# Performance work log

Measured on AMD Instinct MI355X. Metric: run time of the kernel, lower is better.

Reference implementation:

```python
import jax, jax.numpy as jnp
import numpy as np

N = 50000        # nodes
E = 1_600_000    # edges
G = 64           # graphs in batch
IN = 10          # raw node feature width
XS, XE = 4, 10   # bus slice -> in_dim = 6
H = 256          # hidden_dim
OUT = 256        # out_dim
L = 3            # n_layers per expert
NE = 8           # n_experts
K = 2            # top_k


def _w(key, shape):
    fan_in = shape[-2] if len(shape) > 1 else shape[-1]
    return jax.random.normal(key, shape, jnp.float32) / np.sqrt(fan_in).astype(np.float32)


def setup_inputs() -> dict:
    key = jax.random.key(0)
    ks = jax.random.split(key, 18)
    x = jax.random.normal(ks[0], (N, IN), jnp.float32)
    edge_index = jax.random.randint(ks[1], (2, E), 0, N, dtype=jnp.int32)
    batch = jnp.sort(jax.random.randint(ks[2], (N,), 0, G, dtype=jnp.int32))
    return {
        "x": x,
        "edge_index": edge_index,
        "batch": batch,
        # SharedBusEncoder: Linear(in_dim, hidden) + ReLU
        "W_enc": _w(ks[3], (XE - XS, H)), "b_enc": jnp.zeros((H,), jnp.float32),
        # semantic BaseRouter: Linear(H,H)+ReLU+Linear(H,NE)
        "Ws1": _w(ks[4], (H, H)), "bs1": jnp.zeros((H,), jnp.float32),
        "Ws2": _w(ks[5], (H, NE)), "bs2": jnp.zeros((NE,), jnp.float32),
        # structural BaseRouter: Linear(2,H)+ReLU+Linear(H,NE)
        "Wt1": _w(ks[6], (2, H)), "bt1": jnp.zeros((H,), jnp.float32),
        "Wt2": _w(ks[7], (H, NE)), "bt2": jnp.zeros((NE,), jnp.float32),
        # GraphConvExpert stacks: x' = x@W_self + (sum_neighbors x)@W_neigh + b
        "W_self": _w(ks[8], (NE, L, H, OUT)),
        "W_neigh": _w(ks[9], (NE, L, H, OUT)),
        "b_exp": jnp.zeros((NE, L, OUT), jnp.float32),
    }


def reference(x, edge_index, batch, W_enc, b_enc, Ws1, bs1, Ws2, bs2,
              Wt1, bt1, Wt2, bt2, W_self, W_neigh, b_exp):
    src, dst = edge_index[0], edge_index[1]

    # SharedBusEncoder on bus feature slice
    h = jax.nn.relu(x[:, XS:XE] @ W_enc + b_enc)                       # [N, H]

    # graph_size_features: per-graph log node/edge counts, broadcast to nodes
    nodes_per_g = jax.ops.segment_sum(jnp.ones((N,), jnp.float32), batch, G)
    edges_per_g = jax.ops.segment_sum(jnp.ones((E,), jnp.float32), batch[src], G)
    size_feat = jnp.stack([jnp.log1p(nodes_per_g), jnp.log1p(edges_per_g)], -1)[batch]  # [N, 2]

    # dual routers, averaged
    sem = jax.nn.relu(h @ Ws1 + bs1) @ Ws2 + bs2                       # [N, NE]
    stru = jax.nn.relu(size_feat @ Wt1 + bt1) @ Wt2 + bt2              # [N, NE]
    logits = 0.5 * sem + 0.5 * stru

    # sparse_routing: softmax -> top-k mask -> renormalize (eval path, no noise)
    probs = jax.nn.softmax(logits, axis=-1)
    _, topi = jax.lax.top_k(probs, K)                                  # [N, K]
    mask = jnp.zeros_like(probs).at[jnp.arange(N)[:, None], topi].set(1.0)
    sp = probs * mask
    sparse = sp / jnp.sum(sp, axis=-1, keepdims=True)                  # [N, NE]

    # dense GraphConv experts over all nodes
    def run_expert(Ws, Wn, b):
        z = h
        for l in range(L):
            agg = jax.ops.segment_sum(z[src], dst, N)                  # neighbor sum
            z = z @ Ws[l] + agg @ Wn[l] + b[l]
            if l < L - 1:
                z = jax.nn.relu(z)
        return z                                                        # [N, OUT]

    y = jax.vmap(run_expert)(W_self, W_neigh, b_exp)                   # [NE, N, OUT]
    return jnp.einsum('end,ne->nd', y, sparse)                         # [N, OUT]
```

## Files before the change

kernel.cpp:

```cpp
#include <hip/hip_runtime.h>
#include <hip/hip_bf16.h>


#define NN 50000
#define EE 1600000
#define GG 64
#define HH 256
#define NEXP 8
#define LAY 3
#define KD 512
#define MT 128
#define BK 64
#define LST 72

typedef __attribute__((ext_vector_type(8))) short bf16x8;
typedef __attribute__((ext_vector_type(8))) unsigned short u16x8;
typedef __attribute__((ext_vector_type(4))) float f32x4;

__device__ __forceinline__ float bf2f(unsigned short u) {
    union { unsigned int i; float f; } v; v.i = ((unsigned int)u) << 16; return v.f;
}
__device__ __forceinline__ unsigned short f2bf(float f) {
    union { unsigned int i; float f; } v; v.f = f;
    unsigned int r = (v.i + 0x7FFFu + ((v.i >> 16) & 1u)) >> 16;
    return (unsigned short)r;
}

__global__ void encoder_kernel(const float* __restrict__ x, const float* __restrict__ W,
                               const float* __restrict__ b, unsigned short* __restrict__ out) {
    int n = blockIdx.x, j = threadIdx.x;
    float acc = b[j];
#pragma unroll
    for (int i = 0; i < 6; i++) acc += x[n * 10 + 4 + i] * W[i * HH + j];
    acc = fmaxf(acc, 0.f);
    out[(long)n * KD + j] = f2bf(acc);
}

__global__ void pack_experts(const float* __restrict__ Wself, const float* __restrict__ Wneigh,
                             unsigned short* __restrict__ Bt) {
    int idx = blockIdx.x * 256 + threadIdx.x;
    int n = idx & 255; int r = idx >> 8;
    int k = r & 511; r >>= 9;
    int l = r % LAY; int e = r / LAY;
    float v = (k < 256) ? Wself[(((e * LAY + l) * HH) + k) * HH + n]
                        : Wneigh[(((e * LAY + l) * HH) + (k - 256)) * HH + n];
    Bt[(((long)(e * LAY + l) * HH + n) * KD) + k] = f2bf(v);
}

__global__ void pack_ws1(const float* __restrict__ W, unsigned short* __restrict__ Bt) {
    int idx = blockIdx.x * 256 + threadIdx.x;
    int n = idx & 255; int k = idx >> 8;
    Bt[(long)n * HH + k] = f2bf(W[k * HH + n]);
}

__global__ void deg_kernel(const int* __restrict__ src, const int* __restrict__ dst,
                           int* __restrict__ deg, int* __restrict__ outdeg) {
    int e = blockIdx.x * 256 + threadIdx.x;
    if (e < EE) {
        atomicAdd(&deg[dst[e]], 1);
        atomicAdd(&outdeg[src[e]], 1);
    }
}

__global__ void hist_kernel(const int* __restrict__ batch, const int* __restrict__ outdeg,
                            int* __restrict__ ncnt, int* __restrict__ ecnt) {
    __shared__ int hn[GG], he[GG];
    if (threadIdx.x < GG) { hn[threadIdx.x] = 0; he[threadIdx.x] = 0; }
    __syncthreads();
    int i = blockIdx.x * 256 + threadIdx.x;
    if (i < NN) {
        int g = batch[i];
        atomicAdd(&hn[g], 1);
        atomicAdd(&he[g], outdeg[i]);
    }
    __syncthreads();
    if (threadIdx.x < GG) {
        if (hn[threadIdx.x]) atomicAdd(&ncnt[threadIdx.x], hn[threadIdx.x]);
        if (he[threadIdx.x]) atomicAdd(&ecnt[threadIdx.x], he[threadIdx.x]);
    }
}

__global__ void stru_kernel(const int* __restrict__ ncnt, const int* __restrict__ ecnt,
                            const float* __restrict__ Wt1, const float* __restrict__ bt1,
                            const float* __restrict__ Wt2, const float* __restrict__ bt2,
                            float* __restrict__ strug) {
    __shared__ float t[HH];
    int g = blockIdx.x, j = threadIdx.x;
    float nf = log1pf((float)ncnt[g]);
    float ef = log1pf((float)ecnt[g]);
    float v = nf * Wt1[j] + ef * Wt1[HH + j] + bt1[j];
    t[j] = fmaxf(v, 0.f);
    __syncthreads();
    if (j < 8) {
        float sum = bt2[j];
        for (int k = 0; k < HH; k++) sum += t[k] * Wt2[k * 8 + j];
        strug[g * 8 + j] = sum;
    }
}

__global__ void scan_kernel(const int* __restrict__ deg, int* __restrict__ rowstart,
                            int* __restrict__ cursor) {
    __shared__ int wsum[16];
    __shared__ int carry_s;
    int tid = threadIdx.x;
    int wid = tid >> 6, lane = tid & 63;
    if (tid == 0) carry_s = 0;
    __syncthreads();
    for (int base = 0; base < NN; base += 1024) {
        int i = base + tid;
        int v = (i < NN) ? deg[i] : 0;
        int sc = v;
#pragma unroll
        for (int off = 1; off < 64; off <<= 1) {
            int t = __shfl_up(sc, off, 64);
            if (lane >= off) sc += t;
        }
        if (lane == 63) wsum[wid] = sc;
        __syncthreads();
        int carry = carry_s;
        int prev = 0;
        for (int w = 0; w < wid; w++) prev += wsum[w];
        int excl = carry + prev + sc - v;
        if (i < NN) { rowstart[i] = excl; cursor[i] = excl; }
        __syncthreads();
        if (tid == 1023) carry_s = carry + prev + sc;
    }
    __syncthreads();
    if (tid == 0) rowstart[NN] = carry_s;
}

__global__ void scatter_kernel(const int* __restrict__ src, const int* __restrict__ dst,
                               int* __restrict__ cursor, unsigned short* __restrict__ cols) {
    int e = blockIdx.x * 256 + threadIdx.x;
    if (e < EE) {
        int p = atomicAdd(&cursor[dst[e]], 1);
        cols[p] = (unsigned short)src[e];
    }
}

__global__ void agg_kernel(const unsigned short* __restrict__ Z, unsigned short* __restrict__ Aout,
                           const int* __restrict__ rowstart, const unsigned short* __restrict__ cols,
                           const int* __restrict__ list, const int* __restrict__ cntp) {
    int half = threadIdx.x >> 5;
    int lane = threadIdx.x & 31;
    int idx = blockIdx.x * 8 + half;
    int limit = cntp ? *cntp : NN;
    if (idx >= limit) return;
    int nid = list ? list[idx] : idx;
    int s = rowstart[nid], e = rowstart[nid + 1];
    float acc[8] = {0.f, 0.f, 0.f, 0.f, 0.f, 0.f, 0.f, 0.f};
    int i = s;
    for (; i + 8 <= e; i += 8) {
        int c[8];
#pragma unroll
        for (int u = 0; u < 8; u++) c[u] = (int)cols[i + u];
        u16x8 v[8];
#pragma unroll
        for (int u = 0; u < 8; u++) v[u] = *(const u16x8*)&Z[(long)c[u] * KD + lane * 8];
#pragma unroll
        for (int u = 0; u < 8; u++)
#pragma unroll
            for (int j = 0; j < 8; j++) acc[j] += bf2f(v[u][j]);
    }
    for (; i < e; i++) {
        int c = (int)cols[i];
        u16x8 v = *(const u16x8*)&Z[(long)c * KD + lane * 8];
#pragma unroll
        for (int j = 0; j < 8; j++) acc[j] += bf2f(v[j]);
    }
    u16x8 o;
#pragma unroll
    for (int j = 0; j < 8; j++) o[j] = f2bf(acc[j]);
    *(u16x8*)&Aout[(long)nid * KD + 256 + lane * 8] = o;
}

__global__ void route_kernel(const unsigned short* __restrict__ T, const float* __restrict__ Ws2,
                             const float* __restrict__ bs2, const float* __restrict__ strug,
                             const int* __restrict__ batch, float* __restrict__ sparse) {
    int nid = blockIdx.x * 4 + (threadIdx.x >> 6);
    if (nid >= NN) return;
    int lane = threadIdx.x & 63;
    float s[8];
#pragma unroll
    for (int j = 0; j < 8; j++) s[j] = 0.f;
    ushort4 t4 = *(const ushort4*)&T[(long)nid * HH + lane * 4];
    float tv[4] = { bf2f(t4.x), bf2f(t4.y), bf2f(t4.z), bf2f(t4.w) };
#pragma unroll
    for (int kk = 0; kk < 4; kk++) {
        int k = lane * 4 + kk;
#pragma unroll
        for (int j = 0; j < 8; j++) s[j] += tv[kk] * Ws2[k * 8 + j];
    }
#pragma unroll
    for (int off = 32; off >= 1; off >>= 1) {
#pragma unroll
        for (int j = 0; j < 8; j++) s[j] += __shfl_xor(s[j], off, 64);
    }
    int g = batch[nid];
    float p[8], mx = -1e30f;
#pragma unroll
    for (int j = 0; j < 8; j++) {
        p[j] = 0.5f * (s[j] + bs2[j] + strug[g * 8 + j]);
        mx = fmaxf(mx, p[j]);
    }
    float ex[8];
#pragma unroll
    for (int j = 0; j < 8; j++) ex[j] = expf(p[j] - mx);
    int i1 = 0;
#pragma unroll
    for (int j = 1; j < 8; j++) if (ex[j] > ex[i1]) i1 = j;
    int i2 = (i1 == 0) ? 1 : 0;
#pragma unroll
    for (int j = 0; j < 8; j++) if (j != i1 && ex[j] > ex[i2]) i2 = j;
    float r = 1.f / (ex[i1] + ex[i2]);
    if (lane < 8)
        sparse[(long)nid * 8 + lane] = (lane == i1) ? ex[i1] * r : (lane == i2) ? ex[i2] * r : 0.f;
}

__global__ void build_lists(const float* __restrict__ sparse, int* __restrict__ cnt,
                            int* __restrict__ lists) {
    int n = blockIdx.x * 256 + threadIdx.x;
    if (n >= NN) return;
#pragma unroll
    for (int e = 0; e < NEXP; e++) {
        if (sparse[n * 8 + e] > 0.f) {
            int p = atomicAdd(&cnt[e], 1);
            lists[(long)e * NN + p] = n;
        }
    }
}

template <int MODE>
__global__ __launch_bounds__(256, 2) void gemm_kernel(
    const unsigned short* __restrict__ A, int lda, int K,
    const unsigned short* __restrict__ Bt, const float* __restrict__ bias,
    void* __restrict__ outp, int ldz,
    const float* __restrict__ sparse, int expert,
    const int* __restrict__ list, const int* __restrict__ cntp) {
    __shared__ __align__(16) unsigned short Alds[MT * LST];
    __shared__ __align__(16) unsigned short Blds[HH * LST];
    __shared__ int nodeids[MT];
    const int tid = threadIdx.x;
    const int wave = tid >> 6, lane = tid & 63;
    const int m = lane & 15, q = lane >> 4;
    const long row0 = (long)blockIdx.x * MT;

    if constexpr (MODE == 1) {
        int limit = *cntp;
        if (row0 >= limit) return;
        if (tid < MT) {
            long rr = row0 + tid;
            nodeids[tid] = (rr < limit) ? list[rr] : -1;
        }
        __syncthreads();
    }

    f32x4 acc[2][16];
#pragma unroll
    for (int i = 0; i < 2; i++)
#pragma unroll
        for (int j = 0; j < 16; j++) acc[i][j] = (f32x4){0.f, 0.f, 0.f, 0.f};

    for (int k0 = 0; k0 < K; k0 += BK) {
#pragma unroll
        for (int i = 0; i < 4; i++) {
            int chunk = tid + 256 * i;
            int r = chunk >> 3, kc = (chunk & 7) << 3;
            u16x8 v = {0, 0, 0, 0, 0, 0, 0, 0};
            if constexpr (MODE == 0) {
                long grow = row0 + r;
                if (grow < NN) v = *(const u16x8*)&A[grow * lda + k0 + kc];
            } else {
                int nid2 = nodeids[r];
                if (nid2 >= 0) v = *(const u16x8*)&A[(long)nid2 * lda + k0 + kc];
            }
            *(u16x8*)&Alds[r * LST + kc] = v;
        }
#pragma unroll
        for (int i = 0; i < 8; i++) {
            int chunk = tid + 256 * i;
            int nn2 = chunk >> 3, kc = (chunk & 7) << 3;
            u16x8 v = *(const u16x8*)&Bt[(long)nn2 * K + k0 + kc];
            *(u16x8*)&Blds[nn2 * LST + kc] = v;
        }
        __syncthreads();
#pragma unroll
        for (int kk = 0; kk < BK; kk += 32) {
            bf16x8 a0 = *(const bf16x8*)&Alds[(wave * 32 + m) * LST + kk + q * 8];
            bf16x8 a1 = *(const bf16x8*)&Alds[(wave * 32 + 16 + m) * LST + kk + q * 8];
#pragma unroll
            for (int ct = 0; ct < 16; ct++) {
                bf16x8 b = *(const bf16x8*)&Blds[(ct * 16 + m) * LST + kk + q * 8];
                acc[0][ct] = __builtin_amdgcn_mfma_f32_16x16x32_bf16(a0, b, acc[0][ct], 0, 0, 0);
                acc[1][ct] = __builtin_amdgcn_mfma_f32_16x16x32_bf16(a1, b, acc[1][ct], 0, 0, 0);
            }
        }
        __syncthreads();
    }
#pragma unroll
    for (int mt = 0; mt < 2; mt++) {
        int rtile = wave * 32 + mt * 16 + q * 4;
        if constexpr (MODE == 0) {
            long rbase = row0 + rtile;
#pragma unroll
            for (int ct = 0; ct < 16; ct++) {
                int col = ct * 16 + m;
                float bv = bias[col];
#pragma unroll
                for (int r = 0; r < 4; r++) {
                    long grow = rbase + r;
                    if (grow < NN) {
                        float v = fmaxf(acc[mt][ct][r] + bv, 0.f);
                        ((unsigned short*)outp)[grow * ldz + col] = f2bf(v);
                    }
                }
            }
        } else {
            int nid4[4]; float w4[4];
#pragma unroll
            for (int r = 0; r < 4; r++) {
                nid4[r] = nodeids[rtile + r];
                w4[r] = (nid4[r] >= 0) ? sparse[(long)nid4[r] * 8 + expert] : 0.f;
            }
#pragma unroll
            for (int ct = 0; ct < 16; ct++) {
                int col = ct * 16 + m;
                float bv = bias[col];
#pragma unroll
                for (int r = 0; r < 4; r++) {
                    if (nid4[r] >= 0) {
                        float* o = (float*)outp + (long)nid4[r] * HH + col;
                        *o += w4[r] * (acc[mt][ct][r] + bv);
                    }
                }
            }
        }
    }
}

extern "C" void kernel_launch(void* const* d_in, const int* in_sizes, int n_in,
                              void* d_out, int out_size, void* d_ws, size_t ws_size,
                              hipStream_t stream) {
    const float* x     = (const float*)d_in[0];
    const int*   ei    = (const int*)d_in[1];
    const int*   src   = ei;
    const int*   dst   = ei + EE;
    const int*   batch = (const int*)d_in[2];
    const float* W_enc = (const float*)d_in[3];
    const float* b_enc = (const float*)d_in[4];
    const float* Ws1   = (const float*)d_in[5];
    const float* bs1   = (const float*)d_in[6];
    const float* Ws2   = (const float*)d_in[7];
    const float* bs2   = (const float*)d_in[8];
    const float* Wt1   = (const float*)d_in[9];
    const float* bt1   = (const float*)d_in[10];
    const float* Wt2   = (const float*)d_in[11];
    const float* bt2   = (const float*)d_in[12];
    const float* W_self  = (const float*)d_in[13];
    const float* W_neigh = (const float*)d_in[14];
    const float* b_exp   = (const float*)d_in[15];
    float* out = (float*)d_out;

    char* ws = (char*)d_ws;
    size_t off = 0;
    auto alloc = [&](size_t b) { size_t p = off; off = (off + b + 255) & ~(size_t)255; return p; };
    const size_t MPAD = 50048;

    unsigned short* Ash = (unsigned short*)(ws + alloc(MPAD * KD * 2));
    unsigned short* Ab0 = (unsigned short*)(ws + alloc(MPAD * KD * 2));
    unsigned short* Ab1 = (unsigned short*)(ws + alloc(MPAD * KD * 2));
    unsigned short* Tbuf = Ab1;
    unsigned short* BtE = (unsigned short*)(ws + alloc((size_t)NEXP * LAY * HH * KD * 2));
    unsigned short* Bt1 = (unsigned short*)(ws + alloc((size_t)HH * HH * 2));
    float* sparse  = (float*)(ws + alloc((size_t)NN * 8 * 4));
    float* strug   = (float*)(ws + alloc((size_t)GG * 8 * 4));
    int* ncnt      = (int*)(ws + alloc((size_t)GG * 4));
    int* ecnt      = (int*)(ws + alloc((size_t)GG * 4));
    int* deg       = (int*)(ws + alloc((size_t)NN * 4));
    int* outdeg    = (int*)(ws + alloc((size_t)NN * 4));
    int* rowstart  = (int*)(ws + alloc((size_t)(NN + 1) * 4));
    int* cursor    = (int*)(ws + alloc((size_t)NN * 4));
    unsigned short* cols = (unsigned short*)(ws + alloc((size_t)EE * 2));
    int* lists     = (int*)(ws + alloc((size_t)NEXP * NN * 4));
    int* cnt8      = (int*)(ws + alloc((size_t)NEXP * 4));

    hipMemsetAsync(ncnt, 0, GG * 4, stream);
    hipMemsetAsync(ecnt, 0, GG * 4, stream);
    hipMemsetAsync(deg, 0, (size_t)NN * 4, stream);
    hipMemsetAsync(outdeg, 0, (size_t)NN * 4, stream);
    hipMemsetAsync(cnt8, 0, NEXP * 4, stream);
    hipMemsetAsync(out, 0, (size_t)NN * HH * 4, stream);

    pack_experts<<<NEXP * LAY * KD * HH / 256, 256, 0, stream>>>(W_self, W_neigh, BtE);
    pack_ws1<<<HH * HH / 256, 256, 0, stream>>>(Ws1, Bt1);
    encoder_kernel<<<NN, HH, 0, stream>>>(x, W_enc, b_enc, Ash);

    deg_kernel<<<(EE + 255) / 256, 256, 0, stream>>>(src, dst, deg, outdeg);
    hist_kernel<<<(NN + 255) / 256, 256, 0, stream>>>(batch, outdeg, ncnt, ecnt);
    scan_kernel<<<1, 1024, 0, stream>>>(deg, rowstart, cursor);
    scatter_kernel<<<(EE + 255) / 256, 256, 0, stream>>>(src, dst, cursor, cols);
    stru_kernel<<<GG, HH, 0, stream>>>(ncnt, ecnt, Wt1, bt1, Wt2, bt2, strug);

    const int GB = (NN + MT - 1) / MT;
    const int AGB = NN / 8;

    gemm_kernel<0><<<GB, 256, 0, stream>>>(Ash, KD, HH, Bt1, bs1, Tbuf, HH, nullptr, 0,
                                           nullptr, nullptr);
    route_kernel<<<(NN + 3) / 4, 256, 0, stream>>>(Tbuf, Ws2, bs2, strug, batch, sparse);
    build_lists<<<(NN + 255) / 256, 256, 0, stream>>>(sparse, cnt8, lists);

    agg_kernel<<<AGB, 256, 0, stream>>>(Ash, Ash, rowstart, cols, nullptr, nullptr);

    for (int e = 0; e < NEXP; e++) {
        const unsigned short* B0 = BtE + (size_t)(e * LAY + 0) * HH * KD;
        const unsigned short* B1 = BtE + (size_t)(e * LAY + 1) * HH * KD;
        const unsigned short* B2 = BtE + (size_t)(e * LAY + 2) * HH * KD;
        const float* bb = b_exp + (size_t)e * LAY * HH;
        const int* le = lists + (size_t)e * NN;
        gemm_kernel<0><<<GB, 256, 0, stream>>>(Ash, KD, KD, B0, bb, Ab0, KD, nullptr, 0,
                                               nullptr, nullptr);
        agg_kernel<<<AGB, 256, 0, stream>>>(Ab0, Ab0, rowstart, cols, nullptr, nullptr);
        gemm_kernel<0><<<GB, 256, 0, stream>>>(Ab0, KD, KD, B1, bb + HH, Ab1, KD, nullptr, 0,
                                               nullptr, nullptr);
        agg_kernel<<<AGB, 256, 0, stream>>>(Ab1, Ab1, rowstart, cols, le, cnt8 + e);
        gemm_kernel<1><<<GB, 256, 0, stream>>>(Ab1, KD, KD, B2, bb + 2 * HH, out, 0, sparse, e,
                                               le, cnt8 + e);
    }
}
```

Measured before the change: 2.471 ms.

## Pre-swizzle weights into MFMA fragment order, async-load B, read A directly

Weight packing now writes B in per-lane MFMA fragment order, so each 64-wide K tile can be copied into LDS with global_load_lds 16-byte async copies, double-buffered across K steps. The A operand is no longer staged in LDS. Each wave loads its A fragments straight from global memory into registers. Waves are rearranged into a 2x2 grid of 64x128 sub-tiles, which roughly halves per-wave B fragment reads from LDS at the cost of more A register traffic. This removes one of the two barriers per K step and the A staging, but relies on async-copy ordering with only one barrier per iteration and uses 64KB of LDS, which may limit occupancy.

```diff
diff --git a/kernel.cpp b/kernel.cpp
--- a/kernel.cpp
+++ b/kernel.cpp
@@ -10,8 +10,6 @@
 #define LAY 3
 #define KD 512
 #define MT 128
-#define BK 64
-#define LST 72
 
 typedef __attribute__((ext_vector_type(8))) short bf16x8;
 typedef __attribute__((ext_vector_type(8))) unsigned short u16x8;
@@ -25,6 +23,11 @@
     unsigned int r = (v.i + 0x7FFFu + ((v.i >> 16) & 1u)) >> 16;
     return (unsigned short)r;
 }
+__device__ __forceinline__ void async_cp16(const unsigned short* g, unsigned short* l) {
+    __builtin_amdgcn_global_load_lds(
+        (const __attribute__((address_space(1))) unsigned int*)g,
+        (__attribute__((address_space(3))) unsigned int*)l, 16, 0, 0);
+}
 
 __global__ void encoder_kernel(const float* __restrict__ x, const float* __restrict__ W,
                                const float* __restrict__ b, unsigned short* __restrict__ out) {
@@ -40,17 +43,20 @@
                              unsigned short* __restrict__ Bt) {
     int idx = blockIdx.x * 256 + threadIdx.x;
     int n = idx & 255; int r = idx >> 8;
-    int k = r & 511; r >>= 9;
-    int l = r % LAY; int e = r / LAY;
-    float v = (k < 256) ? Wself[(((e * LAY + l) * HH) + k) * HH + n]
-                        : Wneigh[(((e * LAY + l) * HH) + (k - 256)) * HH + n];
-    Bt[(((long)(e * LAY + l) * HH + n) * KD) + k] = f2bf(v);
+    int k = r & 511; int el = r >> 9;
+    float v = (k < 256) ? Wself[((el * 256) + k) * 256 + n]
+                        : Wneigh[((el * 256) + (k - 256)) * 256 + n];
+    int kt = k >> 6, kk = (k >> 5) & 1, q = (k >> 3) & 3, j = k & 7;
+    int ct = n >> 4, mm = n & 15, lane = q * 16 + mm;
+    Bt[(size_t)el * 131072 + (size_t)(kt * 32 + ct * 2 + kk) * 512 + lane * 8 + j] = f2bf(v);
 }
 
 __global__ void pack_ws1(const float* __restrict__ W, unsigned short* __restrict__ Bt) {
     int idx = blockIdx.x * 256 + threadIdx.x;
     int n = idx & 255; int k = idx >> 8;
-    Bt[(long)n * HH + k] = f2bf(W[k * HH + n]);
+    int kt = k >> 6, kk = (k >> 5) & 1, q = (k >> 3) & 3, j = k & 7;
+    int ct = n >> 4, mm = n & 15, lane = q * 16 + mm;
+    Bt[(size_t)(kt * 32 + ct * 2 + kk) * 512 + lane * 8 + j] = f2bf(W[k * HH + n]);
 }
 
 __global__ void deg_kernel(const int* __restrict__ src, const int* __restrict__ dst,
@@ -237,81 +243,92 @@
     void* __restrict__ outp, int ldz,
     const float* __restrict__ sparse, int expert,
     const int* __restrict__ list, const int* __restrict__ cntp) {
-    __shared__ __align__(16) unsigned short Alds[MT * LST];
-    __shared__ __align__(16) unsigned short Blds[HH * LST];
+    __shared__ __align__(16) unsigned short Blds[2][16384];
     __shared__ int nodeids[MT];
     const int tid = threadIdx.x;
     const int wave = tid >> 6, lane = tid & 63;
+    const int wr = wave & 1, wc = wave >> 1;
     const int m = lane & 15, q = lane >> 4;
-    const long row0 = (long)blockIdx.x * MT;
+    const int row0 = blockIdx.x * MT;
+    const int NT = K >> 6;
 
     if constexpr (MODE == 1) {
         int limit = *cntp;
         if (row0 >= limit) return;
         if (tid < MT) {
-            long rr = row0 + tid;
+            int rr = row0 + tid;
             nodeids[tid] = (rr < limit) ? list[rr] : -1;
         }
+    }
+
+    {
+        const unsigned short* g = Bt + (size_t)wave * 4096 + lane * 8;
+        unsigned short* l = &Blds[0][wave * 4096];
+#pragma unroll
+        for (int i = 0; i < 8; i++) async_cp16(g + i * 512, l + i * 512);
+    }
+    if constexpr (MODE == 1) __syncthreads();
+
+    int arow[4];
+#pragma unroll
+    for (int rt = 0; rt < 4; rt++) {
+        int rr = wr * 64 + rt * 16 + m;
+        if constexpr (MODE == 0) {
+            int gr = row0 + rr;
+            arow[rt] = (gr < NN) ? gr : NN - 1;
+        } else {
+            int nid2 = nodeids[rr];
+            arow[rt] = (nid2 >= 0) ? nid2 : 0;
+        }
+    }
+
+    f32x4 acc[4][8];
+#pragma unroll
+    for (int i = 0; i < 4; i++)
+#pragma unroll
+        for (int j = 0; j < 8; j++) acc[i][j] = (f32x4){0.f, 0.f, 0.f, 0.f};
+
+    for (int kt = 0; kt < NT; kt++) {
         __syncthreads();
-    }
-
-    f32x4 acc[2][16];
-#pragma unroll
-    for (int i = 0; i < 2; i++)
-#pragma unroll
-        for (int j = 0; j < 16; j++) acc[i][j] = (f32x4){0.f, 0.f, 0.f, 0.f};
-
-    for (int k0 = 0; k0 < K; k0 += BK) {
-#pragma unroll
-        for (int i = 0; i < 4; i++) {
-            int chunk = tid + 256 * i;
-            int r = chunk >> 3, kc = (chunk & 7) << 3;
-            u16x8 v = {0, 0, 0, 0, 0, 0, 0, 0};
-            if constexpr (MODE == 0) {
-                long grow = row0 + r;
-                if (grow < NN) v = *(const u16x8*)&A[grow * lda + k0 + kc];
-            } else {
-                int nid2 = nodeids[r];
-                if (nid2 >= 0) v = *(const u16x8*)&A[(long)nid2 * lda + k0 + kc];
+        if (kt + 1 < NT) {
+            const unsigned short* g = Bt + (size_t)(kt + 1) * 16384 + wave * 4096 + lane * 8;
+            unsigned short* l = &Blds[(kt + 1) & 1][wave * 4096];
+#pragma unroll
+            for (int i = 0; i < 8; i++) async_cp16(g + i * 512, l + i * 512);
+        }
+        bf16x8 afr[4][2];
+#pragma unroll
+        for (int rt = 0; rt < 4; rt++)
+#pragma unroll
+            for (int kk = 0; kk < 2; kk++)
+                afr[rt][kk] = *(const bf16x8*)&A[(size_t)arow[rt] * lda + kt * 64 + kk * 32 + q * 8];
+        const unsigned short* bb = Blds[kt & 1];
+#pragma unroll
+        for (int kk = 0; kk < 2; kk++)
+#pragma unroll
+            for (int ct = 0; ct < 8; ct++) {
+                bf16x8 bfr = *(const bf16x8*)&bb[(size_t)((wc * 8 + ct) * 2 + kk) * 512 + lane * 8];
+#pragma unroll
+                for (int rt = 0; rt < 4; rt++)
+                    acc[rt][ct] = __builtin_amdgcn_mfma_f32_16x16x32_bf16(afr[rt][kk], bfr,
+                                                                          acc[rt][ct], 0, 0, 0);
             }
-            *(u16x8*)&Alds[r * LST + kc] = v;
-        }
-#pragma unroll
-        for (int i = 0; i < 8; i++) {
-            int chunk = tid + 256 * i;
-            int nn2 = chunk >> 3, kc = (chunk & 7) << 3;
-            u16x8 v = *(const u16x8*)&Bt[(long)nn2 * K + k0 + kc];
-            *(u16x8*)&Blds[nn2 * LST + kc] = v;
-        }
-        __syncthreads();
-#pragma unroll
-        for (int kk = 0; kk < BK; kk += 32) {
-            bf16x8 a0 = *(const bf16x8*)&Alds[(wave * 32 + m) * LST + kk + q * 8];
-            bf16x8 a1 = *(const bf16x8*)&Alds[(wave * 32 + 16 + m) * LST + kk + q * 8];
-#pragma unroll
-            for (int ct = 0; ct < 16; ct++) {
-                bf16x8 b = *(const bf16x8*)&Blds[(ct * 16 + m) * LST + kk + q * 8];
-                acc[0][ct] = __builtin_amdgcn_mfma_f32_16x16x32_bf16(a0, b, acc[0][ct], 0, 0, 0);
-                acc[1][ct] = __builtin_amdgcn_mfma_f32_16x16x32_bf16(a1, b, acc[1][ct], 0, 0, 0);
-            }
-        }
-        __syncthreads();
-    }
-#pragma unroll
-    for (int mt = 0; mt < 2; mt++) {
-        int rtile = wave * 32 + mt * 16 + q * 4;
+    }
+
+#pragma unroll
+    for (int rt = 0; rt < 4; rt++) {
+        int rr0 = wr * 64 + rt * 16 + q * 4;
         if constexpr (MODE == 0) {
-            long rbase = row0 + rtile;
-#pragma unroll
-            for (int ct = 0; ct < 16; ct++) {
-                int col = ct * 16 + m;
+#pragma unroll
+            for (int ct = 0; ct < 8; ct++) {
+                int col = wc * 128 + ct * 16 + m;
                 float bv = bias[col];
 #pragma unroll
                 for (int r = 0; r < 4; r++) {
-                    long grow = rbase + r;
+                    int grow = row0 + rr0 + r;
                     if (grow < NN) {
-                        float v = fmaxf(acc[mt][ct][r] + bv, 0.f);
-                        ((unsigned short*)outp)[grow * ldz + col] = f2bf(v);
+                        float v = fmaxf(acc[rt][ct][r] + bv, 0.f);
+                        ((unsigned short*)outp)[(size_t)grow * ldz + col] = f2bf(v);
                     }
                 }
             }
@@ -319,18 +336,18 @@
             int nid4[4]; float w4[4];
 #pragma unroll
             for (int r = 0; r < 4; r++) {
-                nid4[r] = nodeids[rtile + r];
-                w4[r] = (nid4[r] >= 0) ? sparse[(long)nid4[r] * 8 + expert] : 0.f;
+                nid4[r] = nodeids[rr0 + r];
+                w4[r] = (nid4[r] >= 0) ? sparse[(size_t)nid4[r] * 8 + expert] : 0.f;
             }
 #pragma unroll
-            for (int ct = 0; ct < 16; ct++) {
-                int col = ct * 16 + m;
+            for (int ct = 0; ct < 8; ct++) {
+                int col = wc * 128 + ct * 16 + m;
                 float bv = bias[col];
 #pragma unroll
                 for (int r = 0; r < 4; r++) {
                     if (nid4[r] >= 0) {
-                        float* o = (float*)outp + (long)nid4[r] * HH + col;
-                        *o += w4[r] * (acc[mt][ct][r] + bv);
+                        float* o = (float*)outp + (size_t)nid4[r] * HH + col;
+                        *o += w4[r] * (acc[rt][ct][r] + bv);
                     }
                 }
             }
@@ -412,9 +429,9 @@
     agg_kernel<<<AGB, 256, 0, stream>>>(Ash, Ash, rowstart, cols, nullptr, nullptr);
 
     for (int e = 0; e < NEXP; e++) {
-        const unsigned short* B0 = BtE + (size_t)(e * LAY + 0) * HH * KD;
-        const unsigned short* B1 = BtE + (size_t)(e * LAY + 1) * HH * KD;
-        const unsigned short* B2 = BtE + (size_t)(e * LAY + 2) * HH * KD;
+        const unsigned short* B0 = BtE + (size_t)(e * LAY + 0) * 131072;
+        const unsigned short* B1 = BtE + (size_t)(e * LAY + 1) * 131072;
+        const unsigned short* B2 = BtE + (size_t)(e * LAY + 2) * 131072;
         const float* bb = b_exp + (size_t)e * LAY * HH;
         const int* le = lists + (size_t)e * NN;
         gemm_kernel<0><<<GB, 256, 0, stream>>>(Ash, KD, KD, B0, bb, Ab0, KD, nullptr, 0,
```

After: 2.477 ms. Within noise of the previous version (+0.2%).
